# Kernel optimization log

Measured on AMD Instinct MI355X. Metric: run time of the kernel, lower is better.

Reference implementation:

```python
import jax, jax.numpy as jnp
import numpy as np

N = 50000      # nodes per graph batch (per side)
E = 600000     # edges per side
B = 4096       # number of graphs (drug pairs)
D = 128        # node_dim == hidden_dim
K = 128        # kge_dim
R = 86         # rel_total
L = 3          # n_iter
EPS = 1e-5


def setup_inputs() -> dict:
    key = jax.random.key(0)
    ks = jax.random.split(key, 16)
    inp = {}
    inp["x1"] = jax.random.normal(ks[0], (N, D), jnp.float32)
    inp["x2"] = jax.random.normal(ks[1], (N, D), jnp.float32)
    inp["edge_index1"] = jax.random.randint(ks[2], (2, E), 0, N)
    inp["edge_index2"] = jax.random.randint(ks[3], (2, E), 0, N)
    inp["batch1"] = jnp.sort(jax.random.randint(ks[4], (N,), 0, B))
    inp["batch2"] = jnp.sort(jax.random.randint(ks[5], (N,), 0, B))
    inp["rel"] = jax.random.randint(ks[6], (B,), 0, R)
    # SAGEConv params, stacked over L layers (all [D,D] since node_dim==hidden_dim)
    sc = 0.05
    inp["Wl"] = jax.random.normal(ks[7], (L, D, D), jnp.float32) * sc   # lin on aggregated neighbors (has bias)
    inp["bl"] = jnp.zeros((L, D), jnp.float32)
    inp["Wr"] = jax.random.normal(ks[8], (L, D, D), jnp.float32) * sc   # root (self) lin, no bias
    # BatchNorm (eval mode: running stats)
    inp["bn_gamma"] = jnp.ones((L, D), jnp.float32)
    inp["bn_beta"] = jnp.zeros((L, D), jnp.float32)
    inp["bn_mean"] = jnp.zeros((L, D), jnp.float32)
    inp["bn_var"] = jnp.ones((L, D), jnp.float32)
    # relation embedding + final MLP
    inp["kge"] = jax.random.normal(ks[9], (R, K), jnp.float32)
    inp["W1"] = jax.random.normal(ks[10], (2 * D + K, D), jnp.float32) * sc
    inp["b1"] = jnp.zeros((D,), jnp.float32)
    inp["W2"] = jax.random.normal(ks[11], (D, 1), jnp.float32) * sc
    inp["b2"] = jnp.zeros((1,), jnp.float32)
    return inp


def _gnn(x, edge_index, Wl, bl, Wr, g, b, m, v):
    src, dst = edge_index[0], edge_index[1]
    deg = jax.ops.segment_sum(jnp.ones((E,), x.dtype), dst, num_segments=N)
    deg = jnp.maximum(deg, 1.0)[:, None]
    for i in range(L):
        agg = jax.ops.segment_sum(x[src], dst, num_segments=N) / deg  # mean aggregation
        h = agg @ Wl[i] + bl[i] + x @ Wr[i]                           # SAGEConv
        h = (h - m[i]) * (g[i] / jnp.sqrt(v[i] + EPS)) + b[i]         # BN (eval)
        x = jax.nn.relu(h)                                            # dropout = identity (eval)
    return x


def reference(x1, edge_index1, batch1, x2, edge_index2, batch2, rel,
              Wl, bl, Wr, bn_gamma, bn_beta, bn_mean, bn_var,
              kge, W1, b1, W2, b2):
    h1 = _gnn(x1, edge_index1, Wl, bl, Wr, bn_gamma, bn_beta, bn_mean, bn_var)
    h2 = _gnn(x2, edge_index2, Wl, bl, Wr, bn_gamma, bn_beta, bn_mean, bn_var)
    p1 = jax.ops.segment_sum(h1, batch1, num_segments=B)  # global_add_pool
    p2 = jax.ops.segment_sum(h2, batch2, num_segments=B)
    r = kge[rel]                                          # [B, K]
    z = jnp.concatenate([p1, p2, r], axis=-1)             # [B, 2D+K]
    h = jax.nn.relu(z @ W1 + b1)
    out = h @ W2 + b2
    return out.reshape(-1)
```

## Files before the change

kernel.cpp:

```cpp
#include <hip/hip_runtime.h>

#define NN 50000
#define NE 600000
#define NB 4096
#define DD 128
#define EPSV 1e-5f
#define NBKT 196
#define NCHUNK 256
#define CHSZ ((NE + NCHUNK - 1) / NCHUNK)

typedef __bf16 bf16x8 __attribute__((ext_vector_type(8)));
typedef float f32x4 __attribute__((ext_vector_type(4)));
typedef float f32x2 __attribute__((ext_vector_type(2)));

__device__ inline unsigned short f2bf(float f) {
    unsigned u = __float_as_uint(f);
    u = (u + 0x7FFFu + ((u >> 16) & 1u)) >> 16;
    return (unsigned short)u;
}
__device__ inline float bf2f(unsigned short h) {
    return __uint_as_float(((unsigned)h) << 16);
}

__global__ void k_prep(const float* __restrict__ x1, const float* __restrict__ x2,
                       unsigned short* __restrict__ xh, unsigned short* __restrict__ xl,
                       const float* __restrict__ Wl, const float* __restrict__ Wr,
                       const float* __restrict__ W1,
                       unsigned short* __restrict__ wfp, unsigned* __restrict__ w1p,
                       const int* __restrict__ d0, const int* __restrict__ d1,
                       int* __restrict__ bcnt) {
    __shared__ int h[NBKT];
    int b = blockIdx.x;
    int tid = threadIdx.x;
    if (b < 12500) {
        int i = b * 256 + tid;
        const float* x = (i < NN * 32) ? x1 : x2;
        int j = (i < NN * 32) ? i : i - NN * 32;
        float4 v = ((const float4*)x)[j];
        ushort4 hh, ll;
        hh.x = f2bf(v.x); ll.x = f2bf(v.x - bf2f(hh.x));
        hh.y = f2bf(v.y); ll.y = f2bf(v.y - bf2f(hh.y));
        hh.z = f2bf(v.z); ll.z = f2bf(v.z - bf2f(hh.z));
        hh.w = f2bf(v.w); ll.w = f2bf(v.w - bf2f(hh.w));
        ((ushort4*)xh)[i] = hh;
        ((ushort4*)xl)[i] = ll;
    } else if (b < 12500 + 576) {
        int t = (b - 12500) * 256 + tid;
        if (t < 3 * 128 * 256) {
            int k = t & 255;
            int n = (t >> 8) & 127;
            int l = t >> 15;
            float w = (k < 128) ? Wl[l * 16384 + k * 128 + n] : Wr[l * 16384 + (k - 128) * 128 + n];
            unsigned short hh = f2bf(w);
            unsigned short lo = f2bf(w - bf2f(hh));
            int c = k >> 5, kk = k & 31;
            size_t base = (size_t)l * 65536 + (size_t)c * 8192 + n * 32 + kk;
            wfp[base] = hh;
            wfp[base + 4096] = lo;
        } else if (t < 3 * 128 * 256 + 128 * 384) {
            int u = t - 3 * 128 * 256;
            int n = u / 384;
            int k = u - n * 384;
            float w = W1[k * 128 + n];
            unsigned short hh = f2bf(w);
            unsigned short ll = f2bf(w - bf2f(hh));
            w1p[u] = ((unsigned)hh << 16) | (unsigned)ll;
        }
    } else {
        int hb = b - 13076;
        int side = (hb >= NCHUNK) ? 1 : 0;
        int c = hb - side * NCHUNK;
        const int* dst = side ? d1 : d0;
        for (int i = tid; i < NBKT; i += 256) h[i] = 0;
        __syncthreads();
        int e0 = c * CHSZ, e1 = min(e0 + CHSZ, NE);
        for (int e = e0 + tid; e < e1; e += 256) atomicAdd(&h[dst[e] >> 8], 1);
        __syncthreads();
        int* bc = bcnt + ((size_t)side * NCHUNK + c) * NBKT;
        for (int i = tid; i < NBKT; i += 256) bc[i] = h[i];
    }
}

__global__ void k_s1(int* __restrict__ bcnt, int* __restrict__ btot) {
    int side = (blockIdx.x >= NBKT) ? 1 : 0;
    int b = blockIdx.x - side * NBKT;
    int tid = threadIdx.x;
    int idx = ((size_t)side * NCHUNK + tid) * NBKT + b;
    int v = bcnt[idx];
    int lane = tid & 63, wv = tid >> 6;
    int x = v;
#pragma unroll
    for (int off = 1; off < 64; off <<= 1) {
        int y = __shfl_up(x, off, 64);
        if (lane >= off) x += y;
    }
    __shared__ int ws4[4];
    if (lane == 63) ws4[wv] = x;
    __syncthreads();
    int add = 0;
#pragma unroll
    for (int w = 0; w < 4; w++)
        if (w < wv) add += ws4[w];
    int incl = x + add;
    bcnt[idx] = incl - v;
    if (tid == 255) btot[side * NBKT + b] = incl;
}

__global__ void k_s2(const int* __restrict__ btot, int* __restrict__ bbase,
                     int* __restrict__ ptrC) {
    int side = blockIdx.x;
    int tid = threadIdx.x;
    int v = (tid < NBKT) ? btot[side * NBKT + tid] : 0;
    int lane = tid & 63, wv = tid >> 6;
    int x = v;
#pragma unroll
    for (int off = 1; off < 64; off <<= 1) {
        int y = __shfl_up(x, off, 64);
        if (lane >= off) x += y;
    }
    __shared__ int ws4[4];
    if (lane == 63) ws4[wv] = x;
    __syncthreads();
    int add = 0;
#pragma unroll
    for (int w = 0; w < 4; w++)
        if (w < wv) add += ws4[w];
    int incl = x + add;
    if (tid < NBKT) bbase[side * NBKT + tid] = incl - v;
    if (tid == 0 && side == 1) ptrC[2 * NN] = 2 * NE;
}

__global__ void k_part(const int* __restrict__ s0, const int* __restrict__ d0,
                       const int* __restrict__ s1, const int* __restrict__ d1,
                       const int* __restrict__ bcnt, const int* __restrict__ bbase,
                       int* __restrict__ part) {
    int side = (blockIdx.x >= NCHUNK) ? 1 : 0;
    int c = blockIdx.x - side * NCHUNK;
    const int* src = side ? s1 : s0;
    const int* dst = side ? d1 : d0;
    int tid = threadIdx.x;
    __shared__ int off[NBKT];
    const int* bc = bcnt + ((size_t)side * NCHUNK + c) * NBKT;
    for (int i = tid; i < NBKT; i += 256) off[i] = bbase[side * NBKT + i] + bc[i];
    __syncthreads();
    int e0 = c * CHSZ, e1 = min(e0 + CHSZ, NE);
    int* P = part + (size_t)side * NE;
    int soff = side * NN;
    for (int e = e0 + tid; e < e1; e += 256) {
        int d = dst[e];
        int pos = atomicAdd(&off[d >> 8], 1);
        P[pos] = ((src[e] + soff) << 8) | (d & 255);
    }
}

__global__ void k_csr(const int* __restrict__ part, const int* __restrict__ bbase,
                      int* __restrict__ ptrC, float* __restrict__ invdC,
                      int* __restrict__ csrC) {
    int side = (blockIdx.x >= NBKT) ? 1 : 0;
    int b = blockIdx.x - side * NBKT;
    int tid = threadIdx.x;
    const int* P = part + (size_t)side * NE;
    int base = bbase[side * NBKT + b];
    int endp = (b == NBKT - 1) ? NE : bbase[side * NBKT + b + 1];
    __shared__ int cnt[256];
    cnt[tid] = 0;
    __syncthreads();
    for (int e = base + tid; e < endp; e += 256) atomicAdd(&cnt[P[e] & 255], 1);
    __syncthreads();
    int v = cnt[tid];
    int lane = tid & 63, wv = tid >> 6;
    int x = v;
#pragma unroll
    for (int off = 1; off < 64; off <<= 1) {
        int y = __shfl_up(x, off, 64);
        if (lane >= off) x += y;
    }
    __shared__ int ws4[4];
    if (lane == 63) ws4[wv] = x;
    __syncthreads();
    int add = 0;
#pragma unroll
    for (int w = 0; w < 4; w++)
        if (w < wv) add += ws4[w];
    int excl = x + add - v;
    int node = (b << 8) + tid;
    if (node < NN) {
        ptrC[side * NN + node] = side * NE + base + excl;
        invdC[side * NN + node] = 1.0f / (float)(v > 1 ? v : 1);
    }
    __syncthreads();
    cnt[tid] = excl;
    __syncthreads();
    for (int e = base + tid; e < endp; e += 256) {
        int p = P[e];
        int pos = atomicAdd(&cnt[p & 255], 1);
        csrC[(size_t)side * NE + base + pos] = p >> 8;
    }
}

__global__ void k_gather(const unsigned short* __restrict__ xh, const int* __restrict__ ptr,
                         const int* __restrict__ csr, const float* __restrict__ invd,
                         unsigned short* __restrict__ aggH) {
    int wid = threadIdx.x >> 6;
    int lane = threadIdx.x & 63;
    int q = lane >> 4;
    int c = lane & 15;
    int n = blockIdx.x * 4 + wid;
    if (n >= 2 * NN) return;
    int beg = ptr[n], end = ptr[n + 1];
    float id = invd[n];
    f32x2 a2[4];
#pragma unroll
    for (int k = 0; k < 4; k++) a2[k] = (f32x2){0.f, 0.f};

    for (int base = beg; base < end; base += 64) {
        int cnt = min(end - base, 64);
        int idxv = csr[base + min(lane, cnt - 1)];
        for (int e0 = 0; e0 < cnt; e0 += 8) {
            int eA = e0 + q;
            int eB = e0 + 4 + q;
            int iA = __shfl(idxv, eA, 64);
            int iB = __shfl(idxv, eB, 64);
            f32x2 wA2 = (eA < cnt) ? (f32x2){1.f, 1.f} : (f32x2){0.f, 0.f};
            f32x2 wB2 = (eB < cnt) ? (f32x2){1.f, 1.f} : (f32x2){0.f, 0.f};
            uint4 vA = *(const uint4*)(xh + (((unsigned)iA << 7) + (c << 3)));
            uint4 vB = *(const uint4*)(xh + (((unsigned)iB << 7) + (c << 3)));
            a2[0] += wA2 * (f32x2){__uint_as_float(vA.x << 16), __uint_as_float(vA.x & 0xffff0000u)};
            a2[1] += wA2 * (f32x2){__uint_as_float(vA.y << 16), __uint_as_float(vA.y & 0xffff0000u)};
            a2[2] += wA2 * (f32x2){__uint_as_float(vA.z << 16), __uint_as_float(vA.z & 0xffff0000u)};
            a2[3] += wA2 * (f32x2){__uint_as_float(vA.w << 16), __uint_as_float(vA.w & 0xffff0000u)};
            a2[0] += wB2 * (f32x2){__uint_as_float(vB.x << 16), __uint_as_float(vB.x & 0xffff0000u)};
            a2[1] += wB2 * (f32x2){__uint_as_float(vB.y << 16), __uint_as_float(vB.y & 0xffff0000u)};
            a2[2] += wB2 * (f32x2){__uint_as_float(vB.z << 16), __uint_as_float(vB.z & 0xffff0000u)};
            a2[3] += wB2 * (f32x2){__uint_as_float(vB.w << 16), __uint_as_float(vB.w & 0xffff0000u)};
        }
    }
    float a[8];
    a[0] = a2[0][0]; a[1] = a2[0][1];
    a[2] = a2[1][0]; a[3] = a2[1][1];
    a[4] = a2[2][0]; a[5] = a2[2][1];
    a[6] = a2[3][0]; a[7] = a2[3][1];
#pragma unroll
    for (int k = 0; k < 8; k++) {
        a[k] += __shfl_xor(a[k], 16, 64);
        a[k] += __shfl_xor(a[k], 32, 64);
    }
    if (q == 0) {
        unsigned short h0 = f2bf(a[0] * id), h1 = f2bf(a[1] * id);
        unsigned short h2 = f2bf(a[2] * id), h3 = f2bf(a[3] * id);
        unsigned short h4 = f2bf(a[4] * id), h5 = f2bf(a[5] * id);
        unsigned short h6 = f2bf(a[6] * id), h7 = f2bf(a[7] * id);
        uint4 o;
        o.x = (unsigned)h0 | ((unsigned)h1 << 16);
        o.y = (unsigned)h2 | ((unsigned)h3 << 16);
        o.z = (unsigned)h4 | ((unsigned)h5 << 16);
        o.w = (unsigned)h6 | ((unsigned)h7 << 16);
        *(uint4*)(aggH + (size_t)n * DD + c * 8) = o;
    }
}

__launch_bounds__(256)
__global__ void k_gemmL(const unsigned short* __restrict__ AH,
                        const unsigned short* __restrict__ XH, const unsigned short* __restrict__ XL,
                        const unsigned short* __restrict__ wfp,
                        const float* __restrict__ bl, const float* __restrict__ g,
                        const float* __restrict__ be, const float* __restrict__ mn,
                        const float* __restrict__ vr,
                        unsigned short* __restrict__ OH, unsigned short* __restrict__ OL,
                        float* __restrict__ Of, int f32out) {
    __shared__ __align__(16) unsigned short sBuf[4][128 * 32];
    unsigned short (*sA)[128 * 32] = &sBuf[0];
    unsigned short (*sW)[128 * 32] = &sBuf[2];
    int tid = threadIdx.x;
    int lane = tid & 63, w = tid >> 6;
    int fm = lane & 15, kq = lane >> 4;
    int m0 = blockIdx.x * 128;
    int wr = (w & 1) * 64;
    int wn = (w >> 1) * 64;
    int ksw = kq ^ ((fm >> 1) & 3);

    float scv[4], shv[4];
#pragma unroll
    for (int nt = 0; nt < 4; nt++) {
        int jj = wn + nt * 16 + fm;
        float s = g[jj] * rsqrtf(vr[jj] + EPSV);
        scv[nt] = s;
        shv[nt] = (bl[jj] - mn[jj]) * s + be[jj];
    }

    f32x4 acc[4][4];
#pragma unroll
    for (int i = 0; i < 4; i++)
#pragma unroll
        for (int j = 0; j < 4; j++) acc[i][j] = (f32x4){0.f, 0.f, 0.f, 0.f};

    for (int c = 0; c < 8; c++) {
        int isA = (c < 4);
        if (c > 0) __syncthreads();
        const unsigned short* wb = wfp + (size_t)c * 8192;
#pragma unroll
        for (int i = 0; i < 2; i++) {
            int s = tid + 256 * i;
            int row = s >> 2, seg = s & 3;
            int lo_ = row * 32 + ((seg ^ ((row >> 1) & 3)) << 3);
            int grow = m0 + row;
            size_t gofs = (size_t)grow * DD + (c & 3) * 32 + seg * 8;
            uint4 av = make_uint4(0, 0, 0, 0), lv = make_uint4(0, 0, 0, 0);
            if (grow < 2 * NN) {
                av = *(const uint4*)((isA ? AH : XH) + gofs);
                if (!isA) lv = *(const uint4*)(XL + gofs);
            }
            *(uint4*)&sA[0][lo_] = av;
            if (!isA) *(uint4*)&sA[1][lo_] = lv;
            *(uint4*)&sW[0][lo_] = *(const uint4*)(wb + s * 8);
            *(uint4*)&sW[1][lo_] = *(const uint4*)(wb + 4096 + s * 8);
        }
        __syncthreads();

        bf16x8 ah[4], al[4];
#pragma unroll
        for (int mt = 0; mt < 4; mt++) {
            int r = wr + mt * 16 + fm;
            ah[mt] = *(const bf16x8*)&sA[0][r * 32 + ksw * 8];
            if (!isA) al[mt] = *(const bf16x8*)&sA[1][r * 32 + ksw * 8];
        }
#pragma unroll
        for (int nt = 0; nt < 4; nt++) {
            int nr = wn + nt * 16 + fm;
            bf16x8 wh = *(const bf16x8*)&sW[0][nr * 32 + ksw * 8];
            bf16x8 wl = *(const bf16x8*)&sW[1][nr * 32 + ksw * 8];
#pragma unroll
            for (int mt = 0; mt < 4; mt++) {
                acc[mt][nt] = __builtin_amdgcn_mfma_f32_16x16x32_bf16(ah[mt], wh, acc[mt][nt], 0, 0, 0);
                acc[mt][nt] = __builtin_amdgcn_mfma_f32_16x16x32_bf16(ah[mt], wl, acc[mt][nt], 0, 0, 0);
                if (!isA)
                    acc[mt][nt] = __builtin_amdgcn_mfma_f32_16x16x32_bf16(al[mt], wh, acc[mt][nt], 0, 0, 0);
            }
        }
    }

    unsigned* cb = (unsigned*)sBuf;
    int c8 = tid & 15;
    for (int h = 0; h < 2; h++) {
        __syncthreads();
        if ((w & 1) == h) {
#pragma unroll
            for (int mt = 0; mt < 4; mt++) {
#pragma unroll
                for (int r = 0; r < 4; r++) {
                    int rh = mt * 16 + kq * 4 + r;
#pragma unroll
                    for (int nt = 0; nt < 4; nt++) {
                        int col = wn + nt * 16 + fm;
                        float o = fmaxf(acc[mt][nt][r] * scv[nt] + shv[nt], 0.f);
                        unsigned pv;
                        if (f32out) {
                            pv = __float_as_uint(o);
                        } else {
                            unsigned short hi_ = f2bf(o);
                            pv = ((unsigned)hi_ << 16) | (unsigned)f2bf(o - bf2f(hi_));
                        }
                        cb[rh * 128 + col] = pv;
                    }
                }
            }
        }
        __syncthreads();
        if (f32out) {
#pragma unroll
            for (int j = 0; j < 8; j++) {
                int row = (tid >> 5) + j * 8;
                int grow = m0 + h * 64 + row;
                if (grow < 2 * NN)
                    *(uint4*)&Of[(size_t)grow * DD + (tid & 31) * 4] =
                        *(const uint4*)&cb[row * 128 + (tid & 31) * 4];
            }
        } else {
#pragma unroll
            for (int j = 0; j < 4; j++) {
                int row = (tid >> 4) + j * 16;
                int grow = m0 + h * 64 + row;
                if (grow < 2 * NN) {
                    const unsigned* u = &cb[row * 128 + c8 * 8];
                    uint4 hv, lv2;
                    hv.x = (u[0] >> 16) | (u[1] & 0xFFFF0000u);
                    hv.y = (u[2] >> 16) | (u[3] & 0xFFFF0000u);
                    hv.z = (u[4] >> 16) | (u[5] & 0xFFFF0000u);
                    hv.w = (u[6] >> 16) | (u[7] & 0xFFFF0000u);
                    lv2.x = (u[0] & 0xFFFFu) | (u[1] << 16);
                    lv2.y = (u[2] & 0xFFFFu) | (u[3] << 16);
                    lv2.z = (u[4] & 0xFFFFu) | (u[5] << 16);
                    lv2.w = (u[6] & 0xFFFFu) | (u[7] << 16);
                    *(uint4*)&OH[(size_t)grow * DD + c8 * 8] = hv;
                    *(uint4*)&OL[(size_t)grow * DD + c8 * 8] = lv2;
                }
            }
        }
    }
}

__launch_bounds__(128)
__global__ void k_pool2z(const float* __restrict__ cf, const int* __restrict__ bt1,
                         const int* __restrict__ bt2, const int* __restrict__ rel,
                         const float* __restrict__ kge,
                         unsigned short* __restrict__ zh, unsigned short* __restrict__ zl) {
    int side = (blockIdx.x >= NB) ? 1 : 0;
    int b = blockIdx.x - side * NB;
    const int* batch = side ? bt2 : bt1;
    const float* h = cf + (size_t)side * NN * DD;
    __shared__ int sr[2];
    if (threadIdx.x < 2) {
        int target = b + (int)threadIdx.x;
        int lo = 0, hi = NN;
        while (lo < hi) {
            int mid = (lo + hi) >> 1;
            if (batch[mid] < target) lo = mid + 1; else hi = mid;
        }
        sr[threadIdx.x] = lo;
    }
    __syncthreads();
    int beg = sr[0], end = sr[1];
    int t = threadIdx.x;
    float acc = 0.f;
    for (int r = beg; r < end; r++) acc += h[(size_t)r * DD + t];
    size_t zo = (size_t)b * 384 + side * 128 + t;
    unsigned short hh = f2bf(acc);
    zh[zo] = hh;
    zl[zo] = f2bf(acc - bf2f(hh));
    if (side == 0) {
        float kv = kge[(size_t)rel[b] * 128 + t];
        size_t zk = (size_t)b * 384 + 256 + t;
        unsigned short kh = f2bf(kv);
        zh[zk] = kh;
        zl[zk] = f2bf(kv - bf2f(kh));
    }
}

__launch_bounds__(256)
__global__ void k_mlp2(const unsigned short* __restrict__ zh, const unsigned short* __restrict__ zl,
                       const unsigned* __restrict__ w1p,
                       const float* __restrict__ b1, const float* __restrict__ W2,
                       const float* __restrict__ b2, float* __restrict__ out) {
    __shared__ __align__(16) unsigned short sZ[2][32 * 40];
    __shared__ __align__(16) unsigned short sW[2][128 * 40];
    __shared__ float hpart[32][4];
    int tid = threadIdx.x;
    int m0 = blockIdx.x * 32;
    int lane = tid & 63, w = tid >> 6;
    int fm = lane & 15, q = lane >> 4;
    int wn = w * 32;

    f32x4 acc[2][2];
#pragma unroll
    for (int i = 0; i < 2; i++)
#pragma unroll
        for (int j = 0; j < 2; j++) acc[i][j] = (f32x4){0.f, 0.f, 0.f, 0.f};

    for (int c = 0; c < 12; c++) {
        int k0 = c * 32;
        __syncthreads();
        {
            int row = tid >> 3, seg = tid & 7;
            size_t off = (size_t)(m0 + row) * 384 + k0 + seg * 4;
            *(ushort4*)&sZ[0][row * 40 + seg * 4] = *(const ushort4*)(zh + off);
            *(ushort4*)&sZ[1][row * 40 + seg * 4] = *(const ushort4*)(zl + off);
        }
#pragma unroll
        for (int i = 0; i < 4; i++) {
            int u = tid + 256 * i;
            int row = u >> 3, seg = u & 7;
            uint4 val = *(const uint4*)(w1p + (size_t)row * 384 + k0 + seg * 4);
            ushort4 hi, lo;
            hi.x = val.x >> 16; hi.y = val.y >> 16; hi.z = val.z >> 16; hi.w = val.w >> 16;
            lo.x = val.x & 0xFFFF; lo.y = val.y & 0xFFFF; lo.z = val.z & 0xFFFF; lo.w = val.w & 0xFFFF;
            *(ushort4*)&sW[0][row * 40 + seg * 4] = hi;
            *(ushort4*)&sW[1][row * 40 + seg * 4] = lo;
        }
        __syncthreads();
        bf16x8 zfh[2], zfl[2];
#pragma unroll
        for (int mt = 0; mt < 2; mt++) {
            int r = mt * 16 + fm;
            zfh[mt] = *(const bf16x8*)&sZ[0][r * 40 + q * 8];
            zfl[mt] = *(const bf16x8*)&sZ[1][r * 40 + q * 8];
        }
#pragma unroll
        for (int nt = 0; nt < 2; nt++) {
            int nr = wn + nt * 16 + fm;
            bf16x8 wh = *(const bf16x8*)&sW[0][nr * 40 + q * 8];
            bf16x8 wl = *(const bf16x8*)&sW[1][nr * 40 + q * 8];
#pragma unroll
            for (int mt = 0; mt < 2; mt++) {
                acc[mt][nt] = __builtin_amdgcn_mfma_f32_16x16x32_bf16(zfh[mt], wh, acc[mt][nt], 0, 0, 0);
                acc[mt][nt] = __builtin_amdgcn_mfma_f32_16x16x32_bf16(zfh[mt], wl, acc[mt][nt], 0, 0, 0);
                acc[mt][nt] = __builtin_amdgcn_mfma_f32_16x16x32_bf16(zfl[mt], wh, acc[mt][nt], 0, 0, 0);
            }
        }
    }

    float b1v[2], w2v[2];
#pragma unroll
    for (int nt = 0; nt < 2; nt++) {
        int col = wn + nt * 16 + fm;
        b1v[nt] = b1[col];
        w2v[nt] = W2[col];
    }
#pragma unroll
    for (int mt = 0; mt < 2; mt++) {
#pragma unroll
        for (int r = 0; r < 4; r++) {
            float val = 0.f;
#pragma unroll
            for (int nt = 0; nt < 2; nt++)
                val += fmaxf(acc[mt][nt][r] + b1v[nt], 0.f) * w2v[nt];
#pragma unroll
            for (int m = 1; m < 16; m <<= 1) val += __shfl_xor(val, m, 64);
            if (fm == 0) hpart[mt * 16 + q * 4 + r][w] = val;
        }
    }
    __syncthreads();
    if (tid < 32)
        out[m0 + tid] = hpart[tid][0] + hpart[tid][1] + hpart[tid][2] + hpart[tid][3] + b2[0];
}

extern "C" void kernel_launch(void* const* d_in, const int* in_sizes, int n_in,
                              void* d_out, int out_size, void* d_ws, size_t ws_size,
                              hipStream_t stream) {
    const float* x1  = (const float*)d_in[0];
    const float* x2  = (const float*)d_in[1];
    const int*   ei1 = (const int*)d_in[2];
    const int*   ei2 = (const int*)d_in[3];
    const int*   bt1 = (const int*)d_in[4];
    const int*   bt2 = (const int*)d_in[5];
    const int*   rel = (const int*)d_in[6];
    const float* Wl  = (const float*)d_in[7];
    const float* bl  = (const float*)d_in[8];
    const float* Wr  = (const float*)d_in[9];
    const float* g   = (const float*)d_in[10];
    const float* be  = (const float*)d_in[11];
    const float* mn  = (const float*)d_in[12];
    const float* vr  = (const float*)d_in[13];
    const float* kge = (const float*)d_in[14];
    const float* W1  = (const float*)d_in[15];
    const float* b1v = (const float*)d_in[16];
    const float* W2  = (const float*)d_in[17];
    const float* b2v = (const float*)d_in[18];

    char* ws = (char*)d_ws;
    size_t off = 0;
    auto alloc = [&](size_t bytes) {
        void* p = ws + off;
        off += (bytes + 255) & ~(size_t)255;
        return p;
    };
    const size_t PL = (size_t)2 * NN * DD;
    unsigned short* xbufH = (unsigned short*)alloc(PL * 2);
    unsigned short* xbufL = (unsigned short*)alloc(PL * 2);
    unsigned short* obufH = (unsigned short*)alloc(PL * 2);
    unsigned short* obufL = (unsigned short*)alloc(PL * 2);
    unsigned short* aggH  = (unsigned short*)alloc(PL * 2);
    unsigned short* wfp   = (unsigned short*)alloc((size_t)3 * 65536 * 2);
    unsigned* w1p  = (unsigned*)alloc((size_t)128 * 384 * 4);
    unsigned short* zh = (unsigned short*)alloc((size_t)NB * 384 * 2);
    unsigned short* zl = (unsigned short*)alloc((size_t)NB * 384 * 2);
    int*   bcnt    = (int*)alloc((size_t)2 * NCHUNK * NBKT * 4);
    int*   btot    = (int*)alloc((size_t)2 * NBKT * 4);
    int*   bbase   = (int*)alloc((size_t)2 * NBKT * 4);
    int*   part    = (int*)alloc((size_t)2 * NE * 4);
    int*   ptrC    = (int*)alloc((size_t)(2 * NN + 1) * 4);
    float* invdC   = (float*)alloc((size_t)2 * NN * 4);
    int*   csrC    = (int*)alloc((size_t)2 * NE * 4);
    if (off > ws_size) return;

    float* cf = (float*)obufH;

    const int nbPrep  = 12500 + 576 + 512;
    const int nbNode4 = (2 * NN + 3) / 4;
    const int nbGemmL = (2 * NN + 127) / 128;

    k_prep<<<nbPrep, 256, 0, stream>>>(x1, x2, xbufH, xbufL, Wl, Wr, W1, wfp, w1p,
                                       ei1 + NE, ei2 + NE, bcnt);

    k_s1<<<2 * NBKT, 256, 0, stream>>>(bcnt, btot);
    k_s2<<<2, 256, 0, stream>>>(btot, bbase, ptrC);
    k_part<<<2 * NCHUNK, 256, 0, stream>>>(ei1, ei1 + NE, ei2, ei2 + NE, bcnt, bbase, part);
    k_csr<<<2 * NBKT, 256, 0, stream>>>(part, bbase, ptrC, invdC, csrC);

    k_gather<<<nbNode4, 256, 0, stream>>>(xbufH, ptrC, csrC, invdC, aggH);
    k_gemmL<<<nbGemmL, 256, 0, stream>>>(aggH, xbufH, xbufL, wfp, bl, g, be, mn, vr,
                                         obufH, obufL, (float*)nullptr, 0);
    k_gather<<<nbNode4, 256, 0, stream>>>(obufH, ptrC, csrC, invdC, aggH);
    k_gemmL<<<nbGemmL, 256, 0, stream>>>(aggH, obufH, obufL, wfp + 65536, bl + 128, g + 128,
                                         be + 128, mn + 128, vr + 128,
                                         xbufH, xbufL, (float*)nullptr, 0);
    k_gather<<<nbNode4, 256, 0, stream>>>(xbufH, ptrC, csrC, invdC, aggH);
    k_gemmL<<<nbGemmL, 256, 0, stream>>>(aggH, xbufH, xbufL, wfp + 131072, bl + 256, g + 256,
                                         be + 256, mn + 256, vr + 256,
                                         (unsigned short*)nullptr, (unsigned short*)nullptr, cf, 1);

    k_pool2z<<<2 * NB, 128, 0, stream>>>(cf, bt1, bt2, rel, kge, zh, zl);
    k_mlp2<<<NB / 32, 256, 0, stream>>>(zh, zl, w1p, b1v, W2, b2v, (float*)d_out);
}
```

Baseline: 445.0 us.

## Load GEMM weights directly from fragment-ordered global layout, halve tile rows, unroll gather

The Wl/Wr hi/lo bf16 weights are now written in MFMA-fragment order, so each wave loads its B operands straight from global or L2 into registers instead of staging them through LDS. The GEMM tile drops from 128 to 64 rows per block, which shrinks LDS use and doubles the number of blocks for better occupancy. The neighbor gather is unrolled from 2 to 4 rows in flight per lane group to raise memory-level parallelism. In exchange, every block now re-reads the weights from cache, and the smaller tiles mean more total weight traffic and more per-block overhead.

```diff
diff --git a/kernel.cpp b/kernel.cpp
--- a/kernel.cpp
+++ b/kernel.cpp
@@ -26,7 +26,7 @@
                        unsigned short* __restrict__ xh, unsigned short* __restrict__ xl,
                        const float* __restrict__ Wl, const float* __restrict__ Wr,
                        const float* __restrict__ W1,
-                       unsigned short* __restrict__ wfp, unsigned* __restrict__ w1p,
+                       unsigned short* __restrict__ wf, unsigned* __restrict__ w1p,
                        const int* __restrict__ d0, const int* __restrict__ d1,
                        int* __restrict__ bcnt) {
     __shared__ int h[NBKT];
@@ -53,10 +53,11 @@
             float w = (k < 128) ? Wl[l * 16384 + k * 128 + n] : Wr[l * 16384 + (k - 128) * 128 + n];
             unsigned short hh = f2bf(w);
             unsigned short lo = f2bf(w - bf2f(hh));
-            int c = k >> 5, kk = k & 31;
-            size_t base = (size_t)l * 65536 + (size_t)c * 8192 + n * 32 + kk;
-            wfp[base] = hh;
-            wfp[base + 4096] = lo;
+            int ntile = n >> 4, fm = n & 15, kc = k >> 5, kq = (k & 31) >> 3, j = k & 7;
+            size_t pos = (size_t)l * 65536 + (size_t)(ntile * 8 + kc) * 1024 +
+                         (size_t)(kq * 16 + fm) * 8 + j;
+            wf[pos] = hh;
+            wf[pos + 512] = lo;
         } else if (t < 3 * 128 * 256 + 128 * 384) {
             int u = t - 3 * 128 * 256;
             int n = u / 384;
@@ -216,15 +217,20 @@
     for (int base = beg; base < end; base += 64) {
         int cnt = min(end - base, 64);
         int idxv = csr[base + min(lane, cnt - 1)];
-        for (int e0 = 0; e0 < cnt; e0 += 8) {
-            int eA = e0 + q;
-            int eB = e0 + 4 + q;
+        for (int e0 = 0; e0 < cnt; e0 += 16) {
+            int eA = e0 + q, eB = e0 + 4 + q, eC = e0 + 8 + q, eD = e0 + 12 + q;
             int iA = __shfl(idxv, eA, 64);
             int iB = __shfl(idxv, eB, 64);
+            int iC = __shfl(idxv, eC, 64);
+            int iD = __shfl(idxv, eD, 64);
             f32x2 wA2 = (eA < cnt) ? (f32x2){1.f, 1.f} : (f32x2){0.f, 0.f};
             f32x2 wB2 = (eB < cnt) ? (f32x2){1.f, 1.f} : (f32x2){0.f, 0.f};
+            f32x2 wC2 = (eC < cnt) ? (f32x2){1.f, 1.f} : (f32x2){0.f, 0.f};
+            f32x2 wD2 = (eD < cnt) ? (f32x2){1.f, 1.f} : (f32x2){0.f, 0.f};
             uint4 vA = *(const uint4*)(xh + (((unsigned)iA << 7) + (c << 3)));
             uint4 vB = *(const uint4*)(xh + (((unsigned)iB << 7) + (c << 3)));
+            uint4 vC = *(const uint4*)(xh + (((unsigned)iC << 7) + (c << 3)));
+            uint4 vD = *(const uint4*)(xh + (((unsigned)iD << 7) + (c << 3)));
             a2[0] += wA2 * (f32x2){__uint_as_float(vA.x << 16), __uint_as_float(vA.x & 0xffff0000u)};
             a2[1] += wA2 * (f32x2){__uint_as_float(vA.y << 16), __uint_as_float(vA.y & 0xffff0000u)};
             a2[2] += wA2 * (f32x2){__uint_as_float(vA.z << 16), __uint_as_float(vA.z & 0xffff0000u)};
@@ -233,6 +239,14 @@
             a2[1] += wB2 * (f32x2){__uint_as_float(vB.y << 16), __uint_as_float(vB.y & 0xffff0000u)};
             a2[2] += wB2 * (f32x2){__uint_as_float(vB.z << 16), __uint_as_float(vB.z & 0xffff0000u)};
             a2[3] += wB2 * (f32x2){__uint_as_float(vB.w << 16), __uint_as_float(vB.w & 0xffff0000u)};
+            a2[0] += wC2 * (f32x2){__uint_as_float(vC.x << 16), __uint_as_float(vC.x & 0xffff0000u)};
+            a2[1] += wC2 * (f32x2){__uint_as_float(vC.y << 16), __uint_as_float(vC.y & 0xffff0000u)};
+            a2[2] += wC2 * (f32x2){__uint_as_float(vC.z << 16), __uint_as_float(vC.z & 0xffff0000u)};
+            a2[3] += wC2 * (f32x2){__uint_as_float(vC.w << 16), __uint_as_float(vC.w & 0xffff0000u)};
+            a2[0] += wD2 * (f32x2){__uint_as_float(vD.x << 16), __uint_as_float(vD.x & 0xffff0000u)};
+            a2[1] += wD2 * (f32x2){__uint_as_float(vD.y << 16), __uint_as_float(vD.y & 0xffff0000u)};
+            a2[2] += wD2 * (f32x2){__uint_as_float(vD.z << 16), __uint_as_float(vD.z & 0xffff0000u)};
+            a2[3] += wD2 * (f32x2){__uint_as_float(vD.w << 16), __uint_as_float(vD.w & 0xffff0000u)};
         }
     }
     float a[8];
@@ -260,24 +274,27 @@
 }
 
 __launch_bounds__(256)
-__global__ void k_gemmL(const unsigned short* __restrict__ AH,
+__global__ void k_gemmW(const unsigned short* __restrict__ AH,
                         const unsigned short* __restrict__ XH, const unsigned short* __restrict__ XL,
-                        const unsigned short* __restrict__ wfp,
+                        const unsigned short* __restrict__ wf,
                         const float* __restrict__ bl, const float* __restrict__ g,
                         const float* __restrict__ be, const float* __restrict__ mn,
                         const float* __restrict__ vr,
                         unsigned short* __restrict__ OH, unsigned short* __restrict__ OL,
                         float* __restrict__ Of, int f32out) {
-    __shared__ __align__(16) unsigned short sBuf[4][128 * 32];
-    unsigned short (*sA)[128 * 32] = &sBuf[0];
-    unsigned short (*sW)[128 * 32] = &sBuf[2];
+    __shared__ __align__(16) unsigned short sBuf[8192];
     int tid = threadIdx.x;
     int lane = tid & 63, w = tid >> 6;
     int fm = lane & 15, kq = lane >> 4;
-    int m0 = blockIdx.x * 128;
-    int wr = (w & 1) * 64;
+    int m0 = blockIdx.x * 64;
+    int wr = (w & 1) * 32;
     int wn = (w >> 1) * 64;
     int ksw = kq ^ ((fm >> 1) & 3);
+
+    int srow = tid >> 2, sseg = tid & 3;
+    int ldsoff = srow * 32 + ((sseg ^ ((srow >> 1) & 3)) << 3);
+    bool sok = (m0 + srow) < 2 * NN;
+    size_t gbase = (size_t)(m0 + srow) * DD + sseg * 8;
 
     float scv[4], shv[4];
 #pragma unroll
@@ -288,53 +305,52 @@
         shv[nt] = (bl[jj] - mn[jj]) * s + be[jj];
     }
 
-    f32x4 acc[4][4];
-#pragma unroll
-    for (int i = 0; i < 4; i++)
+    f32x4 acc[2][4];
+#pragma unroll
+    for (int i = 0; i < 2; i++)
 #pragma unroll
         for (int j = 0; j < 4; j++) acc[i][j] = (f32x4){0.f, 0.f, 0.f, 0.f};
 
+    const unsigned short* wfb = wf + (size_t)((w >> 1) * 4) * 8192 + lane * 8;
+
+#pragma unroll
     for (int c = 0; c < 8; c++) {
         int isA = (c < 4);
         if (c > 0) __syncthreads();
-        const unsigned short* wb = wfp + (size_t)c * 8192;
-#pragma unroll
-        for (int i = 0; i < 2; i++) {
-            int s = tid + 256 * i;
-            int row = s >> 2, seg = s & 3;
-            int lo_ = row * 32 + ((seg ^ ((row >> 1) & 3)) << 3);
-            int grow = m0 + row;
-            size_t gofs = (size_t)grow * DD + (c & 3) * 32 + seg * 8;
+        {
             uint4 av = make_uint4(0, 0, 0, 0), lv = make_uint4(0, 0, 0, 0);
-            if (grow < 2 * NN) {
+            size_t gofs = gbase + (size_t)(c & 3) * 32;
+            if (sok) {
                 av = *(const uint4*)((isA ? AH : XH) + gofs);
                 if (!isA) lv = *(const uint4*)(XL + gofs);
             }
-            *(uint4*)&sA[0][lo_] = av;
-            if (!isA) *(uint4*)&sA[1][lo_] = lv;
-            *(uint4*)&sW[0][lo_] = *(const uint4*)(wb + s * 8);
-            *(uint4*)&sW[1][lo_] = *(const uint4*)(wb + 4096 + s * 8);
+            *(uint4*)&sBuf[ldsoff] = av;
+            if (!isA) *(uint4*)&sBuf[2048 + ldsoff] = lv;
+        }
+        bf16x8 wh[4], wl[4];
+#pragma unroll
+        for (int nt = 0; nt < 4; nt++) {
+            const unsigned short* p = wfb + (size_t)(nt * 8 + c) * 1024;
+            wh[nt] = *(const bf16x8*)p;
+            wl[nt] = *(const bf16x8*)(p + 512);
         }
         __syncthreads();
 
-        bf16x8 ah[4], al[4];
-#pragma unroll
-        for (int mt = 0; mt < 4; mt++) {
+        bf16x8 ah[2], al[2];
+#pragma unroll
+        for (int mt = 0; mt < 2; mt++) {
             int r = wr + mt * 16 + fm;
-            ah[mt] = *(const bf16x8*)&sA[0][r * 32 + ksw * 8];
-            if (!isA) al[mt] = *(const bf16x8*)&sA[1][r * 32 + ksw * 8];
+            ah[mt] = *(const bf16x8*)&sBuf[r * 32 + ksw * 8];
+            if (!isA) al[mt] = *(const bf16x8*)&sBuf[2048 + r * 32 + ksw * 8];
         }
 #pragma unroll
         for (int nt = 0; nt < 4; nt++) {
-            int nr = wn + nt * 16 + fm;
-            bf16x8 wh = *(const bf16x8*)&sW[0][nr * 32 + ksw * 8];
-            bf16x8 wl = *(const bf16x8*)&sW[1][nr * 32 + ksw * 8];
-#pragma unroll
-            for (int mt = 0; mt < 4; mt++) {
-                acc[mt][nt] = __builtin_amdgcn_mfma_f32_16x16x32_bf16(ah[mt], wh, acc[mt][nt], 0, 0, 0);
-                acc[mt][nt] = __builtin_amdgcn_mfma_f32_16x16x32_bf16(ah[mt], wl, acc[mt][nt], 0, 0, 0);
+#pragma unroll
+            for (int mt = 0; mt < 2; mt++) {
+                acc[mt][nt] = __builtin_amdgcn_mfma_f32_16x16x32_bf16(ah[mt], wh[nt], acc[mt][nt], 0, 0, 0);
+                acc[mt][nt] = __builtin_amdgcn_mfma_f32_16x16x32_bf16(ah[mt], wl[nt], acc[mt][nt], 0, 0, 0);
                 if (!isA)
-                    acc[mt][nt] = __builtin_amdgcn_mfma_f32_16x16x32_bf16(al[mt], wh, acc[mt][nt], 0, 0, 0);
+                    acc[mt][nt] = __builtin_amdgcn_mfma_f32_16x16x32_bf16(al[mt], wh[nt], acc[mt][nt], 0, 0, 0);
             }
         }
     }
@@ -345,7 +361,7 @@
         __syncthreads();
         if ((w & 1) == h) {
 #pragma unroll
-            for (int mt = 0; mt < 4; mt++) {
+            for (int mt = 0; mt < 2; mt++) {
 #pragma unroll
                 for (int r = 0; r < 4; r++) {
                     int rh = mt * 16 + kq * 4 + r;
@@ -368,18 +384,18 @@
         __syncthreads();
         if (f32out) {
 #pragma unroll
-            for (int j = 0; j < 8; j++) {
+            for (int j = 0; j < 4; j++) {
                 int row = (tid >> 5) + j * 8;
-                int grow = m0 + h * 64 + row;
+                int grow = m0 + h * 32 + row;
                 if (grow < 2 * NN)
                     *(uint4*)&Of[(size_t)grow * DD + (tid & 31) * 4] =
                         *(const uint4*)&cb[row * 128 + (tid & 31) * 4];
             }
         } else {
 #pragma unroll
-            for (int j = 0; j < 4; j++) {
+            for (int j = 0; j < 2; j++) {
                 int row = (tid >> 4) + j * 16;
-                int grow = m0 + h * 64 + row;
+                int grow = m0 + h * 32 + row;
                 if (grow < 2 * NN) {
                     const unsigned* u = &cb[row * 128 + c8 * 8];
                     uint4 hv, lv2;
@@ -559,7 +575,7 @@
     unsigned short* obufH = (unsigned short*)alloc(PL * 2);
     unsigned short* obufL = (unsigned short*)alloc(PL * 2);
     unsigned short* aggH  = (unsigned short*)alloc(PL * 2);
-    unsigned short* wfp   = (unsigned short*)alloc((size_t)3 * 65536 * 2);
+    unsigned short* wf    = (unsigned short*)alloc((size_t)3 * 65536 * 2);
     unsigned* w1p  = (unsigned*)alloc((size_t)128 * 384 * 4);
     unsigned short* zh = (unsigned short*)alloc((size_t)NB * 384 * 2);
     unsigned short* zl = (unsigned short*)alloc((size_t)NB * 384 * 2);
@@ -576,9 +592,9 @@
 
     const int nbPrep  = 12500 + 576 + 512;
     const int nbNode4 = (2 * NN + 3) / 4;
-    const int nbGemmL = (2 * NN + 127) / 128;
-
-    k_prep<<<nbPrep, 256, 0, stream>>>(x1, x2, xbufH, xbufL, Wl, Wr, W1, wfp, w1p,
+    const int nbGemmW = (2 * NN + 63) / 64;
+
+    k_prep<<<nbPrep, 256, 0, stream>>>(x1, x2, xbufH, xbufL, Wl, Wr, W1, wf, w1p,
                                        ei1 + NE, ei2 + NE, bcnt);
 
     k_s1<<<2 * NBKT, 256, 0, stream>>>(bcnt, btot);
@@ -587,14 +603,14 @@
     k_csr<<<2 * NBKT, 256, 0, stream>>>(part, bbase, ptrC, invdC, csrC);
 
     k_gather<<<nbNode4, 256, 0, stream>>>(xbufH, ptrC, csrC, invdC, aggH);
-    k_gemmL<<<nbGemmL, 256, 0, stream>>>(aggH, xbufH, xbufL, wfp, bl, g, be, mn, vr,
+    k_gemmW<<<nbGemmW, 256, 0, stream>>>(aggH, xbufH, xbufL, wf, bl, g, be, mn, vr,
                                          obufH, obufL, (float*)nullptr, 0);
     k_gather<<<nbNode4, 256, 0, stream>>>(obufH, ptrC, csrC, invdC, aggH);
-    k_gemmL<<<nbGemmL, 256, 0, stream>>>(aggH, obufH, obufL, wfp + 65536, bl + 128, g + 128,
+    k_gemmW<<<nbGemmW, 256, 0, stream>>>(aggH, obufH, obufL, wf + 65536, bl + 128, g + 128,
                                          be + 128, mn + 128, vr + 128,
                                          xbufH, xbufL, (float*)nullptr, 0);
     k_gather<<<nbNode4, 256, 0, stream>>>(xbufH, ptrC, csrC, invdC, aggH);
-    k_gemmL<<<nbGemmL, 256, 0, stream>>>(aggH, xbufH, xbufL, wfp + 131072, bl + 256, g + 256,
+    k_gemmW<<<nbGemmW, 256, 0, stream>>>(aggH, xbufH, xbufL, wf + 131072, bl + 256, g + 256,
                                          be + 256, mn + 256, vr + 256,
                                          (unsigned short*)nullptr, (unsigned short*)nullptr, cf, 1);
 
```

After: 420.3 us, median of 3. -5.5%, faster.
